# Kernel tuning notes

Hardware: AMD Instinct MI355X
Metric: run time of the kernel (lower is better)

The kernel has to match this reference:

```python
import math
import jax, jax.numpy as jnp
import numpy as np

B, S, D, H = 4, 1024, 1024, 16


def setup_inputs() -> dict:
    key = jax.random.key(0)
    k1, k2, k3 = jax.random.split(key, 3)
    x = jax.random.normal(k1, (B, S, D), dtype=jnp.float32)
    mask = jnp.ones((B, S), dtype=jnp.int32)  # 1 = valid token (all-ones: see notes)
    W_qkv = jax.random.normal(k2, (D, 3 * D), dtype=jnp.float32) * (1.0 / math.sqrt(D))
    b_qkv = jax.random.normal(k3, (3 * D,), dtype=jnp.float32) * 0.02
    return {"x": x, "mask": mask, "W_qkv": W_qkv, "b_qkv": b_qkv, "num_heads": H}


def reference(x, mask, W_qkv, b_qkv, num_heads):
    Bb, Ss, Dd = x.shape
    head_dim = Dd // num_heads
    scale = 1.0 / math.sqrt(Dd / num_heads)  # matches 1/sqrt(embed_dim/num_heads)

    qkv = x @ W_qkv + b_qkv                                  # [B,S,3D]
    q, k, v = jnp.split(qkv, 3, axis=-1)                      # each [B,S,D]
    q = q.reshape(Bb, Ss, num_heads, head_dim).transpose(0, 2, 1, 3) * scale  # [B,H,S,d]
    k = k.reshape(Bb, Ss, num_heads, head_dim).transpose(0, 2, 1, 3)          # [B,H,S,d]
    v = v.reshape(Bb, Ss, num_heads, head_dim).transpose(0, 2, 1, 3)          # [B,H,S,d]

    attn = jnp.einsum('bhqd,bhkd->bhqk', q, k)                # [B,H,S,S]
    mf = mask.astype(attn.dtype)
    attn_mask = mf[:, None, :, None] * mf[:, None, None, :]   # [B,1,S,S] outer product
    attn = jnp.where(attn_mask == 0, -jnp.inf, attn)
    attn = jax.nn.softmax(attn, axis=-1)

    out = jnp.einsum('bhqk,bhkd->bhqd', attn, v)              # [B,H,S,d]
    return out.transpose(0, 2, 1, 3).reshape(Bb, Ss, Dd)      # [B,S,D]
```

## Files before the change

### kernel.cpp

```cpp
#include <hip/hip_runtime.h>
#include <hip/hip_bf16.h>

typedef __attribute__((ext_vector_type(8))) short short8;
typedef __attribute__((ext_vector_type(4))) float floatx4;

#define MFMA16(A, B, C) __builtin_amdgcn_mfma_f32_16x16x32_bf16(A, B, C, 0, 0, 0)

static constexpr int S  = 1024;
static constexpr int D  = 1024;
static constexpr int N3 = 3 * D;
#define QSCALE 0.18033688011112042f

static inline __device__ ushort f2b(float f) {
  __hip_bfloat16 h = __float2bfloat16(f);
  return *(ushort*)&h;
}

static inline __device__ void gld16(const ushort* g, ushort* l) {
  __builtin_amdgcn_global_load_lds((const __attribute__((address_space(1))) void*)g,
                                   (__attribute__((address_space(3))) void*)l, 16, 0, 0);
}

__global__ __launch_bounds__(256) void prep(const float* __restrict__ x,
                                            const float* __restrict__ w,
                                            ushort* __restrict__ xb,
                                            ushort* __restrict__ wt) {
  __shared__ float t[32][33];
  const int bid = blockIdx.x;
  if (bid < 4096) {
    const int i = (bid * 256 + threadIdx.x) * 4;
    const float4 f = *(const float4*)(x + i);
    ushort4 u;
    u.x = f2b(f.x); u.y = f2b(f.y); u.z = f2b(f.z); u.w = f2b(f.w);
    *(ushort4*)(xb + i) = u;
  } else {
    const int id = bid - 4096;
    const int tx = threadIdx.x & 31;
    const int ty = threadIdx.x >> 5;
    const int n0 = (id % 96) * 32;
    const int k0 = (id / 96) * 32;
#pragma unroll
    for (int j = 0; j < 4; ++j)
      t[ty + j * 8][tx] = w[(long)(k0 + ty + j * 8) * N3 + n0 + tx];
    __syncthreads();
#pragma unroll
    for (int j = 0; j < 4; ++j)
      wt[(long)(n0 + ty + j * 8) * D + k0 + tx] = f2b(t[tx][ty + j * 8]);
  }
}

__global__ __launch_bounds__(512, 2) void qkv_gemm8(const ushort* __restrict__ xb,
                                                    const ushort* __restrict__ wtb,
                                                    const float* __restrict__ bias,
                                                    ushort* __restrict__ Qb,
                                                    ushort* __restrict__ Kb,
                                                    ushort* __restrict__ Vt) {
  __shared__ __align__(16) ushort lds[65536];

  const int tid  = threadIdx.x;
  const int lane = tid & 63;
  const int wid  = tid >> 6;
  const int l15  = lane & 15;
  const int quad = lane >> 4;

  int bid = blockIdx.x;
  bid = (bid & 7) * 24 + (bid >> 3);
  const int n0 = (bid % 12) * 256;
  const int m0 = (bid / 12) * 256;

  const int wr = wid >> 2;
  const int wc = wid & 3;
  const int sz = (l15 & 7) * 8;
  const int cbs_u = (((lane & 7) ^ ((lane >> 3) & 7))) * 8;
  const int srcrow = wid * 8 + (lane >> 3);

  floatx4 acc[8][4];
#pragma unroll
  for (int i = 0; i < 8; ++i)
#pragma unroll
    for (int j = 0; j < 4; ++j) acc[i][j] = (floatx4)0.0f;

  auto stage_g = [&](int g) {
    const int tau = g >> 2, part = g & 3, ab = part & 1, ht = part >> 1;
    const ushort* s0 = ab ? (wtb + (long)(n0 + ht * 128) * D)
                          : (xb  + (long)(m0 + ht * 128) * D);
    const ushort* src = s0 + tau * 64 + cbs_u + (long)srcrow * D;
    ushort* dst = &lds[(tau & 1) * 32768 + ab * 16384 + ht * 8192 + wid * 512];
    gld16(src, dst);
    gld16(src + 64 * D, dst + 4096);
  };

  short8 fa[4][2];
  short8 fb[2][2][2];

  auto LDA = [&](int cb, int mh) {
#pragma unroll
    for (int i = 0; i < 4; ++i)
#pragma unroll
      for (int kk = 0; kk < 2; ++kk)
        fa[i][kk] = *(const short8*)&lds[cb + wr * 8192 +
            (((((mh * 4 + i) * 16 + l15) * 64) + kk * 32 + quad * 8) ^ sz)];
  };
  auto LDB = [&](int cb, int nh) {
#pragma unroll
    for (int j = 0; j < 2; ++j)
#pragma unroll
      for (int kk = 0; kk < 2; ++kk)
        fb[nh][j][kk] = *(const short8*)&lds[cb + 16384 + (wc >> 1) * 8192 +
            ((((((wc & 1) * 64 + (nh * 2 + j) * 16 + l15)) * 64) + kk * 32 + quad * 8) ^ sz)];
  };
  auto MM = [&](int mh, int nh) {
#pragma unroll
    for (int i = 0; i < 4; ++i)
#pragma unroll
      for (int j = 0; j < 2; ++j)
#pragma unroll
        for (int kk = 0; kk < 2; ++kk)
          acc[mh * 4 + i][nh * 2 + j] =
              MFMA16(fa[i][kk], fb[nh][j][kk], acc[mh * 4 + i][nh * 2 + j]);
  };

#pragma unroll
  for (int g = 0; g < 7; ++g) stage_g(g);
  asm volatile("s_waitcnt vmcnt(6)" ::: "memory");
  asm volatile("s_barrier" ::: "memory");

#pragma unroll 2
  for (int kt = 0; kt < 16; ++kt) {
    const int cb = (kt & 1) * 32768;
    LDA(cb, 0); LDB(cb, 0);
    { const int g = kt * 4 + 7; if (g < 64) stage_g(g); }
    asm volatile("s_barrier" ::: "memory");
    asm volatile("s_waitcnt lgkmcnt(0)" ::: "memory");
    __builtin_amdgcn_s_setprio(1); MM(0, 0); __builtin_amdgcn_s_setprio(0);
    asm volatile("s_barrier" ::: "memory");
    LDB(cb, 1);
    asm volatile("s_barrier" ::: "memory");
    asm volatile("s_waitcnt lgkmcnt(0)" ::: "memory");
    __builtin_amdgcn_s_setprio(1); MM(0, 1); __builtin_amdgcn_s_setprio(0);
    asm volatile("s_barrier" ::: "memory");
    LDA(cb, 1);
    { const int g = kt * 4 + 9; if (g < 64) stage_g(g); }
    asm volatile("s_barrier" ::: "memory");
    asm volatile("s_waitcnt lgkmcnt(0)" ::: "memory");
    __builtin_amdgcn_s_setprio(1); MM(1, 1); __builtin_amdgcn_s_setprio(0);
    asm volatile("s_barrier" ::: "memory");
    { const int g = kt * 4 + 8;  if (g < 64) stage_g(g); }
    { const int g = kt * 4 + 10; if (g < 64) stage_g(g); }
    asm volatile("s_barrier" ::: "memory");
    __builtin_amdgcn_s_setprio(1); MM(1, 0); __builtin_amdgcn_s_setprio(0);
    if (kt == 14)      asm volatile("s_waitcnt vmcnt(0)" ::: "memory");
    else if (kt < 14)  asm volatile("s_waitcnt vmcnt(6)" ::: "memory");
    asm volatile("s_barrier" ::: "memory");
  }

  const int cls = n0 >> 10;
#pragma unroll
  for (int ntl = 0; ntl < 4; ++ntl) {
    const int n = n0 + wc * 64 + ntl * 16 + l15;
    const float bv = bias[n];
    if (cls == 0) {
#pragma unroll
      for (int mtl = 0; mtl < 8; ++mtl)
#pragma unroll
        for (int r = 0; r < 4; ++r) {
          const int m = m0 + wr * 128 + mtl * 16 + quad * 4 + r;
          Qb[(long)m * D + n] = f2b((acc[mtl][ntl][r] + bv) * QSCALE);
        }
    } else if (cls == 1) {
#pragma unroll
      for (int mtl = 0; mtl < 8; ++mtl)
#pragma unroll
        for (int r = 0; r < 4; ++r) {
          const int m = m0 + wr * 128 + mtl * 16 + quad * 4 + r;
          Kb[(long)m * D + (n - 1024)] = f2b(acc[mtl][ntl][r] + bv);
        }
    } else {
      const int nn = n - 2048;
      const int hh = nn >> 6, dd = nn & 63;
#pragma unroll
      for (int mtl = 0; mtl < 8; ++mtl) {
        const int m = m0 + wr * 128 + mtl * 16 + quad * 4;
        const int bb = m >> 10, ss = m & 1023;
        ushort4 pk;
        pk.x = f2b(acc[mtl][ntl][0] + bv);
        pk.y = f2b(acc[mtl][ntl][1] + bv);
        pk.z = f2b(acc[mtl][ntl][2] + bv);
        pk.w = f2b(acc[mtl][ntl][3] + bv);
        *(ushort4*)&Vt[((long)(bb * 16 + hh) * 64 + dd) * (long)S + ss] = pk;
      }
    }
  }
}

__global__ __launch_bounds__(256, 4) void attn(const ushort* __restrict__ Qb,
                                               const ushort* __restrict__ Kb,
                                               const ushort* __restrict__ Vt,
                                               float* __restrict__ out) {
  __shared__ __align__(16) ushort Ksm[2][2][64][32];
  __shared__ __align__(16) ushort Vsm[2][2][64][32];
  __shared__ __align__(16) ushort Psm[4][16][64];

  const int tid  = threadIdx.x;
  const int lane = tid & 63;
  const int wid  = tid >> 6;
  const int l15  = lane & 15;
  const int quad = lane >> 4;
  const int bh = blockIdx.x;
  const int qt = blockIdx.y;
  const int b  = bh >> 4;
  const int h  = bh & 15;

  short8 qb[2];
  const int qbase = b * S + qt * 64 + wid * 16;
  {
    const ushort* qp = Qb + (long)(qbase + l15) * D + h * 64;
    qb[0] = *(const short8*)(qp + quad * 8);
    qb[1] = *(const short8*)(qp + 32 + quad * 8);
  }

  floatx4 o[4];
#pragma unroll
  for (int mt = 0; mt < 4; ++mt) o[mt] = (floatx4)0.0f;
  float ppart = 0.f;

  const ushort* kbase = Kb + (long)(b * S) * D + h * 64;
  const ushort* vbase = Vt + (long)(b * 16 + h) * 64 * (long)S;
  const int srow = lane >> 2;
  const int scol = (lane & 3) * 8;
  const int rb = wid * 16;

  auto stage = [&](int kt, int buf) {
#pragma unroll
    for (int kh = 0; kh < 2; ++kh)
      gld16(kbase + (long)(kt * 64 + rb + srow) * D + kh * 32 + scol,
            &Ksm[buf][kh][rb][0]);
#pragma unroll
    for (int kh = 0; kh < 2; ++kh)
      gld16(vbase + (long)(rb + srow) * S + kt * 64 + kh * 32 + scol,
            &Vsm[buf][kh][rb][0]);
  };

  const int swz = l15 & 7;

  stage(0, 0);
  for (int kt = 0; kt < 16; ++kt) {
    const int cur = kt & 1;
    if (kt < 15) {
      stage(kt + 1, cur ^ 1);
      asm volatile("s_waitcnt vmcnt(4)" ::: "memory");
    } else {
      asm volatile("s_waitcnt vmcnt(0)" ::: "memory");
    }
    asm volatile("s_barrier" ::: "memory");

    floatx4 s[4];
#pragma unroll
    for (int mt = 0; mt < 4; ++mt) s[mt] = (floatx4)0.0f;
    __builtin_amdgcn_s_setprio(1);
#pragma unroll
    for (int ks = 0; ks < 2; ++ks)
#pragma unroll
      for (int mt = 0; mt < 4; ++mt) {
        const short8 ka = *(const short8*)&Ksm[cur][ks][mt * 16 + l15][quad * 8];
        s[mt] = MFMA16(ka, qb[ks], s[mt]);
      }
    __builtin_amdgcn_s_setprio(0);

#pragma unroll
    for (int mt = 0; mt < 4; ++mt) {
      const float p0 = exp2f(s[mt][0]);
      const float p1 = exp2f(s[mt][1]);
      const float p2 = exp2f(s[mt][2]);
      const float p3 = exp2f(s[mt][3]);
      ppart += (p0 + p1) + (p2 + p3);
      ushort4 pw;
      pw.x = f2b(p0); pw.y = f2b(p1); pw.z = f2b(p2); pw.w = f2b(p3);
      const int slot = (mt * 2 + (quad >> 1)) ^ swz;
      *(ushort4*)&Psm[wid][l15][slot * 8 + (quad & 1) * 4] = pw;
    }
    asm volatile("s_waitcnt lgkmcnt(0)" ::: "memory");

    short8 pb[2];
#pragma unroll
    for (int ks = 0; ks < 2; ++ks)
      pb[ks] = *(const short8*)&Psm[wid][l15][((ks * 4 + quad) ^ swz) * 8];
    __builtin_amdgcn_s_setprio(1);
#pragma unroll
    for (int ks = 0; ks < 2; ++ks)
#pragma unroll
      for (int mt = 0; mt < 4; ++mt) {
        const short8 va = *(const short8*)&Vsm[cur][ks][mt * 16 + l15][quad * 8];
        o[mt] = MFMA16(va, pb[ks], o[mt]);
      }
    __builtin_amdgcn_s_setprio(0);
    asm volatile("s_barrier" ::: "memory");
  }

  {
    float li = ppart;
    li += __shfl_xor(li, 16);
    li += __shfl_xor(li, 32);
    const float inv = 1.0f / li;
    const int q = qbase + l15;
    const long obase = (long)q * D + h * 64;
#pragma unroll
    for (int mt = 0; mt < 4; ++mt) {
      float4 f;
      f.x = o[mt][0] * inv; f.y = o[mt][1] * inv;
      f.z = o[mt][2] * inv; f.w = o[mt][3] * inv;
      *(float4*)&out[obase + mt * 16 + quad * 4] = f;
    }
  }
}

extern "C" void kernel_launch(void* const* d_in, const int* in_sizes, int n_in,
                              void* d_out, int out_size, void* d_ws, size_t ws_size,
                              hipStream_t stream) {
  const float* x    = (const float*)d_in[0];
  const float* w    = (const float*)d_in[2];
  const float* bias = (const float*)d_in[3];

  ushort* xb  = (ushort*)d_ws;
  ushort* wtb = xb + (long)4096 * 1024;
  ushort* Qb  = wtb + (long)3072 * 1024;
  ushort* Kb  = Qb + (long)4096 * 1024;
  ushort* Vt  = Kb + (long)4096 * 1024;

  prep<<<7168, 256, 0, stream>>>(x, w, xb, wtb);
  qkv_gemm8<<<192, 512, 0, stream>>>(xb, wtb, bias, Qb, Kb, Vt);
  attn<<<dim3(64, 16), 256, 0, stream>>>(Qb, Kb, Vt, (float*)d_out);
}
```

Baseline: 155.2 us.

## Software-pipeline attention loop: overlap PV of previous tile with QK of current

Restructures the attention inner loop so the P·V MFMAs for tile i-1 run in the same phase as the Q·K MFMAs for tile i. K and V staging are split so V loads trail K by one iteration, and the P buffer in shared memory is double-buffered. The aim is to hide the exp/convert and the LDS round-trip for P behind matrix work, and to drop one lgkmcnt wait. Shared memory use grows and launch bounds drop from 4 to 3 blocks per CU, which may reduce occupancy.

```diff
diff --git a/kernel.cpp b/kernel.cpp
--- a/kernel.cpp
+++ b/kernel.cpp
@@ -193,13 +193,13 @@
   }
 }
 
-__global__ __launch_bounds__(256, 4) void attn(const ushort* __restrict__ Qb,
+__global__ __launch_bounds__(256, 3) void attn(const ushort* __restrict__ Qb,
                                                const ushort* __restrict__ Kb,
                                                const ushort* __restrict__ Vt,
                                                float* __restrict__ out) {
   __shared__ __align__(16) ushort Ksm[2][2][64][32];
   __shared__ __align__(16) ushort Vsm[2][2][64][32];
-  __shared__ __align__(16) ushort Psm[4][16][64];
+  __shared__ __align__(16) ushort Psm[2][4][16][64];
 
   const int tid  = threadIdx.x;
   const int lane = tid & 63;
@@ -229,30 +229,37 @@
   const int srow = lane >> 2;
   const int scol = (lane & 3) * 8;
   const int rb = wid * 16;
-
-  auto stage = [&](int kt, int buf) {
+  const int swz = l15 & 7;
+
+  auto stageK = [&](int kt, int buf) {
 #pragma unroll
     for (int kh = 0; kh < 2; ++kh)
       gld16(kbase + (long)(kt * 64 + rb + srow) * D + kh * 32 + scol,
             &Ksm[buf][kh][rb][0]);
+  };
+  auto stageV = [&](int kt, int buf) {
 #pragma unroll
     for (int kh = 0; kh < 2; ++kh)
       gld16(vbase + (long)(rb + srow) * S + kt * 64 + kh * 32 + scol,
             &Vsm[buf][kh][rb][0]);
   };
 
-  const int swz = l15 & 7;
-
-  stage(0, 0);
-  for (int kt = 0; kt < 16; ++kt) {
-    const int cur = kt & 1;
-    if (kt < 15) {
-      stage(kt + 1, cur ^ 1);
-      asm volatile("s_waitcnt vmcnt(4)" ::: "memory");
-    } else {
-      asm volatile("s_waitcnt vmcnt(0)" ::: "memory");
-    }
-    asm volatile("s_barrier" ::: "memory");
+  stageK(0, 0);
+  for (int i = 0; i < 16; ++i) {
+    const int ck = i & 1;
+    const int cv = (i - 1) & 1;
+    if (i < 15) stageK(i + 1, (i + 1) & 1);
+    stageV(i, i & 1);
+    if (i < 15) asm volatile("s_waitcnt vmcnt(4)" ::: "memory");
+    else        asm volatile("s_waitcnt vmcnt(2)" ::: "memory");
+    asm volatile("s_barrier" ::: "memory");
+
+    short8 pb[2];
+    if (i) {
+#pragma unroll
+      for (int ks = 0; ks < 2; ++ks)
+        pb[ks] = *(const short8*)&Psm[cv][wid][l15][((ks * 4 + quad) ^ swz) * 8];
+    }
 
     floatx4 s[4];
 #pragma unroll
@@ -262,9 +269,18 @@
     for (int ks = 0; ks < 2; ++ks)
 #pragma unroll
       for (int mt = 0; mt < 4; ++mt) {
-        const short8 ka = *(const short8*)&Ksm[cur][ks][mt * 16 + l15][quad * 8];
+        const short8 ka = *(const short8*)&Ksm[ck][ks][mt * 16 + l15][quad * 8];
         s[mt] = MFMA16(ka, qb[ks], s[mt]);
       }
+    if (i) {
+#pragma unroll
+      for (int ks = 0; ks < 2; ++ks)
+#pragma unroll
+        for (int mt = 0; mt < 4; ++mt) {
+          const short8 va = *(const short8*)&Vsm[cv][ks][mt * 16 + l15][quad * 8];
+          o[mt] = MFMA16(va, pb[ks], o[mt]);
+        }
+    }
     __builtin_amdgcn_s_setprio(0);
 
 #pragma unroll
@@ -277,24 +293,25 @@
       ushort4 pw;
       pw.x = f2b(p0); pw.y = f2b(p1); pw.z = f2b(p2); pw.w = f2b(p3);
       const int slot = (mt * 2 + (quad >> 1)) ^ swz;
-      *(ushort4*)&Psm[wid][l15][slot * 8 + (quad & 1) * 4] = pw;
-    }
-    asm volatile("s_waitcnt lgkmcnt(0)" ::: "memory");
-
+      *(ushort4*)&Psm[i & 1][wid][l15][slot * 8 + (quad & 1) * 4] = pw;
+    }
+    asm volatile("s_barrier" ::: "memory");
+  }
+
+  asm volatile("s_waitcnt vmcnt(0)" ::: "memory");
+  asm volatile("s_barrier" ::: "memory");
+  {
     short8 pb[2];
 #pragma unroll
     for (int ks = 0; ks < 2; ++ks)
-      pb[ks] = *(const short8*)&Psm[wid][l15][((ks * 4 + quad) ^ swz) * 8];
-    __builtin_amdgcn_s_setprio(1);
+      pb[ks] = *(const short8*)&Psm[15 & 1][wid][l15][((ks * 4 + quad) ^ swz) * 8];
 #pragma unroll
     for (int ks = 0; ks < 2; ++ks)
 #pragma unroll
       for (int mt = 0; mt < 4; ++mt) {
-        const short8 va = *(const short8*)&Vsm[cur][ks][mt * 16 + l15][quad * 8];
+        const short8 va = *(const short8*)&Vsm[15 & 1][ks][mt * 16 + l15][quad * 8];
         o[mt] = MFMA16(va, pb[ks], o[mt]);
       }
-    __builtin_amdgcn_s_setprio(0);
-    asm volatile("s_barrier" ::: "memory");
   }
 
   {
```

After: 164.5 us. +6.0%, slower.
